# Kernel optimization log

Hardware: AMD Instinct MI355X
Metric: run time of the kernel (lower is better)

The kernel has to match this reference:

```python
import jax, jax.numpy as jnp
import numpy as np
import math

B, L = 2048, 60
D, H, NL = 80, 8, 3
HD = D // H            # head_dim = 10
NLOC, NUSR = 1187, 46
DFF = 2 * D
IN_DIM = D + 24 + 32 + 2   # loc(80)+user(24)+weekday(16)+hour(16)+2 continuous


def _ln(x, g, b):
    m = jnp.mean(x, -1, keepdims=True)
    v = jnp.mean((x - m) ** 2, -1, keepdims=True)
    return (x - m) * jax.lax.rsqrt(v + 1e-5) * g + b


def setup_inputs():
    key = jax.random.key(0)
    k = lambda i: jax.random.fold_in(key, i)
    g = lambda i, shp, s: jax.random.normal(k(i), shp, dtype=jnp.float32) * s
    inp = {
        "loc_seq": jax.random.randint(k(0), (B, L), 0, NLOC),
        "user_seq": jax.random.randint(k(1), (B, L), 0, NUSR),
        "weekday_seq": jax.random.randint(k(2), (B, L), 0, 8),
        "start_min_seq": jax.random.randint(k(3), (B, L), 0, 1440),
        "dur_seq": jax.random.randint(k(4), (B, L), 0, 600),
        "diff_seq": jax.random.randint(k(5), (B, L), 0, 100),
        "seq_len": jax.random.randint(k(6), (B,), 1, L + 1),
    }
    # embedding tables (padding_idx=0 rows zeroed where the module uses it)
    inp["loc_table"] = g(10, (NLOC, D), 0.02).at[0].set(0.0)
    inp["user_table"] = g(11, (NUSR, 24), 0.02).at[0].set(0.0)
    inp["wk_table"] = g(12, (8, 16), 0.02).at[0].set(0.0)
    inp["hr_table"] = g(13, (25, 16), 0.02)
    inp["in_w"] = g(14, (IN_DIM, D), 0.09)
    inp["in_b"] = jnp.zeros((D,), jnp.float32)
    inp["in_g"] = jnp.ones((D,), jnp.float32)
    inp["in_be"] = jnp.zeros((D,), jnp.float32)
    inp["pos_emb"] = g(15, (1, L, D), 0.02)
    # per-layer stacked params (NL=3 layers)
    inp["qkv_w"] = g(16, (NL, D, 3 * D), 0.09)
    inp["proj_w"] = g(17, (NL, D, D), 0.11)
    inp["proj_b"] = jnp.zeros((NL, D), jnp.float32)
    inp["rel_emb"] = g(18, (NL, 2 * L - 1, HD), 1.0)
    inp["n1_g"] = jnp.ones((NL, D), jnp.float32)
    inp["n1_b"] = jnp.zeros((NL, D), jnp.float32)
    inp["ffn_w1"] = g(19, (NL, D, DFF), 0.09)
    inp["ffn_b1"] = jnp.zeros((NL, DFF), jnp.float32)
    inp["ffn_w2"] = g(20, (NL, DFF, D), 0.09)
    inp["ffn_b2"] = jnp.zeros((NL, D), jnp.float32)
    inp["n2_g"] = jnp.ones((NL, D), jnp.float32)
    inp["n2_b"] = jnp.zeros((NL, D), jnp.float32)
    inp["fn_g"] = jnp.ones((D,), jnp.float32)
    inp["fn_b"] = jnp.zeros((D,), jnp.float32)
    inp["pr_w1"] = g(21, (D, D), 0.11)
    inp["pr_b1"] = jnp.zeros((D,), jnp.float32)
    inp["pr_w2"] = g(22, (D, NLOC), 0.04)
    inp["pr_b2"] = jnp.zeros((NLOC,), jnp.float32)
    inp["protos"] = g(23, (NLOC, D), 0.04)
    inp["temp"] = jnp.asarray(2.0, jnp.float32)
    return inp


def reference(loc_seq, user_seq, weekday_seq, start_min_seq, dur_seq, diff_seq, seq_len,
              loc_table, user_table, wk_table, hr_table, in_w, in_b, in_g, in_be, pos_emb,
              qkv_w, proj_w, proj_b, rel_emb, n1_g, n1_b, ffn_w1, ffn_b1, ffn_w2, ffn_b2,
              n2_g, n2_b, fn_g, fn_b, pr_w1, pr_b1, pr_w2, pr_b2, protos, temp):
    Bx, Lx = loc_seq.shape
    loc_e = loc_table[loc_seq]                                            # [B,L,80]
    user_e = jnp.broadcast_to(user_table[user_seq[:, 0]][:, None, :], (Bx, Lx, 24))
    hour = jnp.clip(start_min_seq // 60, 0, 23)
    cont = jnp.stack([diff_seq.astype(jnp.float32) / 10.0,
                      dur_seq.astype(jnp.float32) / 300.0], -1)           # [B,L,2]
    x = jnp.concatenate([loc_e, user_e, wk_table[weekday_seq], hr_table[hour], cont], -1)
    x = _ln(x @ in_w + in_b, in_g, in_be) + pos_emb[:, :Lx, :]
    key_mask = loc_seq == 0                                               # mask keys [B,L]
    pos_idx = jnp.arange(Lx)[None, :] - jnp.arange(Lx)[:, None] + (Lx - 1)  # [L,L]
    scale = 1.0 / math.sqrt(HD)
    for l in range(NL):
        qkv = (x @ qkv_w[l]).reshape(Bx, Lx, 3, H, HD)
        q = qkv[:, :, 0].transpose(0, 2, 1, 3)                            # [B,H,L,hd]
        kk = qkv[:, :, 1].transpose(0, 2, 1, 3)
        v = qkv[:, :, 2].transpose(0, 2, 1, 3)
        rel = rel_emb[l][pos_idx]                                         # [L,L,hd]
        attn = (jnp.einsum('bhid,bhjd->bhij', q, kk)
                + jnp.einsum('bhid,ijd->bhij', q, rel)) * scale
        attn = jnp.where(key_mask[:, None, None, :], -jnp.inf, attn)
        a = jax.nn.softmax(attn, -1)
        o = jnp.einsum('bhij,bhjd->bhid', a, v).transpose(0, 2, 1, 3).reshape(Bx, Lx, D)
        x = _ln(x + o @ proj_w[l] + proj_b[l], n1_g[l], n1_b[l])
        f = jax.nn.gelu(x @ ffn_w1[l] + ffn_b1[l], approximate=False) @ ffn_w2[l] + ffn_b2[l]
        x = _ln(x + f, n2_g[l], n2_b[l])
    x = _ln(x, fn_g, fn_b)
    final = x[jnp.arange(Bx), jnp.clip(seq_len - 1, 0, Lx - 1)]           # [B,80]
    logits_param = jax.nn.gelu(final @ pr_w1 + pr_b1, approximate=False) @ pr_w2 + pr_b2
    fnorm = final / jnp.maximum(jnp.linalg.norm(final, axis=-1, keepdims=True), 1e-12)
    pnorm = protos / jnp.maximum(jnp.linalg.norm(protos, axis=-1, keepdims=True), 1e-12)
    logits = 0.5 * logits_param + 0.5 * (fnorm @ pnorm.T) * 15.0
    return logits / jnp.clip(temp, 0.5, 3.0)
```

## Files before the change

### kernel.cpp

```cpp
#include <hip/hip_runtime.h>
#include <hip/hip_bf16.h>
#include <math.h>

#define BB   2048
#define LL   60
#define DD   80
#define HH   8
#define HDD  10
#define NLNUM 3
#define NLOC 1187
#define DFF  160
#define IN_DIM 138
#define RELN 119
#define SCS  68
#define XP   21
#define HP   41
#define VP   35
#define TS   65

__device__ __forceinline__ float gelu_f(float a) {
  float x = fabsf(a) * 0.70710678118654752f;
  float t = 1.0f / (1.0f + 0.3275911f * x);
  float y = t * (0.254829592f + t * (-0.284496736f + t * (1.421413741f +
            t * (-1.453152027f + t * 1.061405429f))));
  float e = 1.0f - y * __expf(-x * x);
  float erf_s = copysignf(e, a);
  return 0.5f * a * (1.0f + erf_s);
}

__global__ __launch_bounds__(256) void k_rprep(
    const float* __restrict__ rel_emb, float* __restrict__ relTg) {
  int idx = blockIdx.x * 256 + threadIdx.x;
  if (idx >= 3600) return;
  int p = idx % 120;
  int d = (idx / 120) % 10;
  int l = idx / 1200;
  float v = 0.0f;
  if (p < RELN) v = rel_emb[l * RELN * HDD + p * HDD + d];
  relTg[idx] = v;
}

__global__ __launch_bounds__(256) void k_embed(
    const int* __restrict__ loc_seq, const int* __restrict__ user_seq,
    const int* __restrict__ wk_seq, const int* __restrict__ sm_seq,
    const int* __restrict__ dur_seq, const int* __restrict__ diff_seq,
    const float* __restrict__ loc_table, const float* __restrict__ user_table,
    const float* __restrict__ wk_table, const float* __restrict__ hr_table,
    const float* __restrict__ in_w, const float* __restrict__ in_b,
    const float* __restrict__ in_g, const float* __restrict__ in_be,
    const float* __restrict__ pos_emb, float* __restrict__ x) {
  int tok0 = blockIdx.x * 48, tid = threadIdx.x;
  __shared__ __align__(16) float vin[48 * VP * 4];
  __shared__ __align__(16) float ws[140 * 80];
  __shared__ float mstd[96];

  float4* vin4 = (float4*)vin;
  float4* ws4  = (float4*)ws;

  for (int i = tid; i < 140 * 20; i += 256) {
    int r = i / 20, c = i % 20;
    float4 v = make_float4(0.0f, 0.0f, 0.0f, 0.0f);
    if (r < IN_DIM) v = *(const float4*)(in_w + r * 80 + c * 4);
    ws4[i] = v;
  }
  for (int i = tid; i < 48 * 35; i += 256) {
    int t = i / 35, s = i % 35;
    int tok = tok0 + t;
    float4 v;
    if (s < 20) {
      int loc = loc_seq[tok];
      v = *(const float4*)(loc_table + (size_t)loc * 80 + s * 4);
    } else if (s < 26) {
      int usr = user_seq[(tok / LL) * LL];
      v = *(const float4*)(user_table + usr * 24 + (s - 20) * 4);
    } else if (s < 30) {
      int wk = wk_seq[tok];
      v = *(const float4*)(wk_table + wk * 16 + (s - 26) * 4);
    } else if (s < 34) {
      int hr = sm_seq[tok] / 60; hr = min(max(hr, 0), 23);
      v = *(const float4*)(hr_table + hr * 16 + (s - 30) * 4);
    } else {
      v.x = (float)diff_seq[tok] / 10.0f;
      v.y = (float)dur_seq[tok] / 300.0f;
      v.z = 0.0f; v.w = 0.0f;
    }
    vin4[t * VP + s] = v;
  }
  __syncthreads();

  int tg = tid / 20, cg = tid % 20, t0 = tg * 4;
  float acc[4][4] = {};
  if (tid < 240) {
    #pragma unroll 7
    for (int iq = 0; iq < 35; iq++) {
      float4 xv[4], wv[4];
      #pragma unroll
      for (int dt = 0; dt < 4; dt++) xv[dt] = vin4[(t0 + dt) * VP + iq];
      #pragma unroll
      for (int di = 0; di < 4; di++) wv[di] = ws4[(iq * 4 + di) * 20 + cg];
      #pragma unroll
      for (int dt = 0; dt < 4; dt++) {
        const float* xp = (const float*)&xv[dt];
        #pragma unroll
        for (int di = 0; di < 4; di++) {
          const float* wp = (const float*)&wv[di];
          #pragma unroll
          for (int dc = 0; dc < 4; dc++) acc[dt][dc] += xp[di] * wp[dc];
        }
      }
    }
  }
  __syncthreads();
  if (tid < 240) {
    float4 bb = *(const float4*)(in_b + cg * 4);
    const float* bp = (const float*)&bb;
    #pragma unroll
    for (int dt = 0; dt < 4; dt++) {
      float4 y;
      y.x = acc[dt][0] + bp[0];
      y.y = acc[dt][1] + bp[1];
      y.z = acc[dt][2] + bp[2];
      y.w = acc[dt][3] + bp[3];
      vin4[(t0 + dt) * VP + cg] = y;
    }
  }
  __syncthreads();
  if (tid < 48) {
    float s = 0.0f, s2 = 0.0f;
    #pragma unroll
    for (int iq = 0; iq < 20; iq++) {
      float4 v = vin4[tid * VP + iq];
      s  += v.x + v.y + v.z + v.w;
      s2 += v.x * v.x + v.y * v.y + v.z * v.z + v.w * v.w;
    }
    float mean = s / 80.0f;
    float var  = fmaxf(s2 / 80.0f - mean * mean, 0.0f);
    mstd[tid] = mean; mstd[48 + tid] = rsqrtf(var + 1e-5f);
  }
  __syncthreads();
  for (int e = tid; e < 960; e += 256) {
    int t = e / 20, c4 = e % 20;
    float4 v = vin4[t * VP + c4];
    float4 gg = *(const float4*)(in_g + c4 * 4);
    float4 bb = *(const float4*)(in_be + c4 * 4);
    float4 pe = *(const float4*)(pos_emb + ((tok0 + t) % LL) * 80 + c4 * 4);
    float m = mstd[t], r = mstd[48 + t];
    float4 out;
    out.x = (v.x - m) * r * gg.x + bb.x + pe.x;
    out.y = (v.y - m) * r * gg.y + bb.y + pe.y;
    out.z = (v.z - m) * r * gg.z + bb.z + pe.z;
    out.w = (v.w - m) * r * gg.w + bb.w + pe.w;
    ((float4*)(x + (size_t)tok0 * 80))[e] = out;
  }
}

__global__ __launch_bounds__(256) void k_qkv(
    const float* __restrict__ x, const float* __restrict__ qkv_w,
    float* __restrict__ qkvo) {
  int b = blockIdx.x, tid = threadIdx.x;
  __shared__ __align__(16) float xsT[20 * TS * 4];
  __shared__ __align__(16) float ws[80 * 60];

  const float4* xb4 = (const float4*)(x + (size_t)b * 4800);
  float4* xsT4 = (float4*)xsT;
  float4* ws4  = (float4*)ws;
  for (int i = tid; i < 1200; i += 256) {
    int t = i / 20, iq = i % 20;
    xsT4[iq * TS + t] = xb4[i];
  }

  for (int c0 = 0; c0 < 240; c0 += 60) {
    __syncthreads();
    for (int i = tid; i < 1200; i += 256)
      ws4[i] = *(const float4*)(qkv_w + (i / 15) * 240 + c0 + (i % 15) * 4);
    __syncthreads();
    if (tid < 225) {
      int tg = tid % 15, cg = tid / 15;
      int t0 = tg * 4;
      float acc[4][4] = {};
      #pragma unroll 5
      for (int iq = 0; iq < 20; iq++) {
        float4 xv[4], wv[4];
        #pragma unroll
        for (int dt = 0; dt < 4; dt++) xv[dt] = xsT4[iq * TS + t0 + dt];
        #pragma unroll
        for (int di = 0; di < 4; di++) wv[di] = ws4[(iq * 4 + di) * 15 + cg];
        #pragma unroll
        for (int dt = 0; dt < 4; dt++) {
          const float* xp = (const float*)&xv[dt];
          #pragma unroll
          for (int di = 0; di < 4; di++) {
            const float* wp = (const float*)&wv[di];
            #pragma unroll
            for (int dc = 0; dc < 4; dc++) acc[dt][dc] += xp[di] * wp[dc];
          }
        }
      }
      float* qb = qkvo + (size_t)b * 14400 + (size_t)(c0 + cg * 4) * 60 + t0;
      #pragma unroll
      for (int dc = 0; dc < 4; dc++)
        *(float4*)(qb + dc * 60) =
            make_float4(acc[0][dc], acc[1][dc], acc[2][dc], acc[3][dc]);
    }
  }
}

__global__ __launch_bounds__(256) void k_attn(
    const float* __restrict__ qkvo, const int* __restrict__ loc_seq,
    const float* __restrict__ relTg,
    float* __restrict__ o) {
  int bh = blockIdx.x;
  int b = bh >> 3, h = bh & 7;
  int tid = threadIdx.x;

  __shared__ __align__(16) float qs[HDD * 60];
  __shared__ __align__(16) float ks[HDD * 60];
  __shared__ __align__(16) float vs[HDD * 60];
  __shared__ __align__(16) float relT[HDD * 120];
  __shared__ __align__(16) float sc[60 * SCS];
  __shared__ __align__(16) float rsum[64];
  __shared__ float msk[60];

  const float4* src = (const float4*)(qkvo + (size_t)b * 14400);
  float4* q4 = (float4*)qs; float4* k4 = (float4*)ks; float4* v4 = (float4*)vs;
  for (int i = tid; i < 150; i += 256) {
    q4[i] = src[h * 150 + i];
    k4[i] = src[1200 + h * 150 + i];
    v4[i] = src[2400 + h * 150 + i];
  }
  const float4* rg4 = (const float4*)relTg;
  float4* relT4 = (float4*)relT;
  for (int i = tid; i < 300; i += 256) relT4[i] = rg4[i];
  if (tid < 60) msk[tid] = (loc_seq[b * LL + tid] == 0) ? 1.0f : 0.0f;
  __syncthreads();

  if (tid < 225) {
    int ig = tid / 15, jg = tid % 15;
    int i0 = ig * 4, j0 = jg * 4;
    int w0 = j0 - i0 + 56;
    float acc[4][4] = {};
    #pragma unroll
    for (int d = 0; d < 10; d++) {
      float4 qv = *(const float4*)(qs + d * 60 + i0);
      float4 kv = *(const float4*)(ks + d * 60 + j0);
      float4 rA = *(const float4*)(relT + d * 120 + w0);
      float4 rB = *(const float4*)(relT + d * 120 + w0 + 4);
      float rr[8] = {rA.x, rA.y, rA.z, rA.w, rB.x, rB.y, rB.z, rB.w};
      const float* qp = (const float*)&qv;
      const float* kp = (const float*)&kv;
      #pragma unroll
      for (int di = 0; di < 4; di++)
        #pragma unroll
        for (int dj = 0; dj < 4; dj++)
          acc[di][dj] += qp[di] * (kp[dj] + rr[dj - di + 3]);
    }
    const float scale = 0.31622776601683794f;
    #pragma unroll
    for (int di = 0; di < 4; di++) {
      #pragma unroll
      for (int dj = 0; dj < 4; dj++) {
        float v = acc[di][dj] * scale;
        if (msk[j0 + dj] != 0.0f) v = -1e30f;
        acc[di][dj] = v;
      }
      *(float4*)(sc + (i0 + di) * SCS + j0) =
          make_float4(acc[di][0], acc[di][1], acc[di][2], acc[di][3]);
    }
  }
  __syncthreads();

  if (tid < 60) {
    float* row = sc + tid * SCS;
    int c = (tid >> 3) & 7;
    float m0 = -3.0e38f, m1 = -3.0e38f, m2 = -3.0e38f, m3 = -3.0e38f;
    #pragma unroll
    for (int s = 0; s < 15; s++) {
      int k = c + s; if (k >= 15) k -= 15;
      float4 v = *(const float4*)(row + 4 * k);
      m0 = fmaxf(m0, v.x); m1 = fmaxf(m1, v.y);
      m2 = fmaxf(m2, v.z); m3 = fmaxf(m3, v.w);
    }
    float m = fmaxf(fmaxf(m0, m1), fmaxf(m2, m3));
    float s0 = 0.0f, s1 = 0.0f, s2 = 0.0f, s3 = 0.0f;
    #pragma unroll
    for (int s = 0; s < 15; s++) {
      int k = c + s; if (k >= 15) k -= 15;
      float4 v = *(float4*)(row + 4 * k);
      v.x = __expf(v.x - m); v.y = __expf(v.y - m);
      v.z = __expf(v.z - m); v.w = __expf(v.w - m);
      *(float4*)(row + 4 * k) = v;
      s0 += v.x; s1 += v.y; s2 += v.z; s3 += v.w;
    }
    rsum[tid] = 1.0f / (s0 + s1 + s2 + s3);
  }
  __syncthreads();

  if (tid < 150) {
    int ig = tid / 10, d = tid % 10;
    float acc[4] = {0, 0, 0, 0};
    #pragma unroll 5
    for (int jq = 0; jq < 15; jq++) {
      float4 vv = *(const float4*)(vs + d * 60 + jq * 4);
      #pragma unroll
      for (int di = 0; di < 4; di++) {
        float4 av = *(const float4*)(sc + (ig + 15 * di) * SCS + jq * 4);
        acc[di] += av.x * vv.x + av.y * vv.y + av.z * vv.z + av.w * vv.w;
      }
    }
    #pragma unroll
    for (int di = 0; di < 4; di++) {
      float r = rsum[ig + 15 * di];
      o[((size_t)b * 60 + ig + 15 * di) * 80 + h * 10 + d] = acc[di] * r;
    }
  }
}

__global__ __launch_bounds__(256) void k_pffn(
    const float* __restrict__ o, const float* __restrict__ proj_w,
    const float* __restrict__ proj_b, const float* __restrict__ g1,
    const float* __restrict__ be1,
    const float* __restrict__ w1, const float* __restrict__ b1,
    const float* __restrict__ w2, const float* __restrict__ b2,
    const float* __restrict__ g2, const float* __restrict__ be2,
    float* __restrict__ x) {
  int tok0 = blockIdx.x * 48, tid = threadIdx.x;
  __shared__ __align__(16) float ys[48 * XP * 4];
  __shared__ __align__(16) float hs[48 * HP * 4];
  __shared__ __align__(16) float ws[80 * 80];
  __shared__ float mstd[96];

  float4* ys4 = (float4*)ys;
  float4* hs4 = (float4*)hs;
  float4* os4 = (float4*)hs;
  float4* ws4 = (float4*)ws;

  const float4* ob4 = (const float4*)(o + (size_t)tok0 * 80);
  for (int i = tid; i < 960; i += 256) os4[(i / 20) * XP + (i % 20)] = ob4[i];
  for (int i = tid; i < 1600; i += 256)
    ws4[i] = *(const float4*)(proj_w + (i / 20) * 80 + (i % 20) * 4);
  __syncthreads();

  int tg = tid / 20, cg = tid % 20, t0 = tg * 4;
  {
    float acc[4][4] = {};
    if (tid < 240) {
      #pragma unroll
      for (int iq = 0; iq < 20; iq++) {
        float4 xv[4], wv[4];
        #pragma unroll
        for (int dt = 0; dt < 4; dt++) xv[dt] = os4[(t0 + dt) * XP + iq];
        #pragma unroll
        for (int di = 0; di < 4; di++) wv[di] = ws4[(iq * 4 + di) * 20 + cg];
        #pragma unroll
        for (int dt = 0; dt < 4; dt++) {
          const float* xp = (const float*)&xv[dt];
          #pragma unroll
          for (int di = 0; di < 4; di++) {
            const float* wp = (const float*)&wv[di];
            #pragma unroll
            for (int dc = 0; dc < 4; dc++) acc[dt][dc] += xp[di] * wp[dc];
          }
        }
      }
      float4 pb = *(const float4*)(proj_b + cg * 4);
      const float* pbp = (const float*)&pb;
      #pragma unroll
      for (int dt = 0; dt < 4; dt++) {
        float4 xr = *(const float4*)(x + (size_t)(tok0 + t0 + dt) * 80 + cg * 4);
        const float* xrp = (const float*)&xr;
        float4 out;
        out.x = acc[dt][0] + pbp[0] + xrp[0];
        out.y = acc[dt][1] + pbp[1] + xrp[1];
        out.z = acc[dt][2] + pbp[2] + xrp[2];
        out.w = acc[dt][3] + pbp[3] + xrp[3];
        ys4[(t0 + dt) * XP + cg] = out;
      }
    }
  }
  __syncthreads();
  if (tid < 48) {
    float s = 0.0f, s2 = 0.0f;
    #pragma unroll
    for (int iq = 0; iq < 20; iq++) {
      float4 v = ys4[tid * XP + iq];
      s  += v.x + v.y + v.z + v.w;
      s2 += v.x * v.x + v.y * v.y + v.z * v.z + v.w * v.w;
    }
    float mean = s / 80.0f;
    float var  = fmaxf(s2 / 80.0f - mean * mean, 0.0f);
    mstd[tid] = mean; mstd[48 + tid] = rsqrtf(var + 1e-5f);
  }
  __syncthreads();
  for (int e = tid; e < 960; e += 256) {
    int t = e / 20, c4 = e % 20;
    float4 v = ys4[t * XP + c4];
    float4 gg = *(const float4*)(g1 + c4 * 4);
    float4 bb = *(const float4*)(be1 + c4 * 4);
    float m = mstd[t], r = mstd[48 + t];
    v.x = (v.x - m) * r * gg.x + bb.x;
    v.y = (v.y - m) * r * gg.y + bb.y;
    v.z = (v.z - m) * r * gg.z + bb.z;
    v.w = (v.w - m) * r * gg.w + bb.w;
    ys4[t * XP + c4] = v;
  }

  for (int c0 = 0; c0 < 160; c0 += 80) {
    __syncthreads();
    for (int i = tid; i < 1600; i += 256)
      ws4[i] = *(const float4*)(w1 + (i / 20) * 160 + c0 + (i % 20) * 4);
    __syncthreads();
    if (tid < 240) {
      float acc[4][4] = {};
      #pragma unroll
      for (int iq = 0; iq < 20; iq++) {
        float4 xv[4], wv[4];
        #pragma unroll
        for (int dt = 0; dt < 4; dt++) xv[dt] = ys4[(t0 + dt) * XP + iq];
        #pragma unroll
        for (int di = 0; di < 4; di++) wv[di] = ws4[(iq * 4 + di) * 20 + cg];
        #pragma unroll
        for (int dt = 0; dt < 4; dt++) {
          const float* xp = (const float*)&xv[dt];
          #pragma unroll
          for (int di = 0; di < 4; di++) {
            const float* wp = (const float*)&wv[di];
            #pragma unroll
            for (int dc = 0; dc < 4; dc++) acc[dt][dc] += xp[di] * wp[dc];
          }
        }
      }
      float4 bb = *(const float4*)(b1 + c0 + cg * 4);
      const float* bp = (const float*)&bb;
      #pragma unroll
      for (int dt = 0; dt < 4; dt++) {
        float4 out;
        float* op = (float*)&out;
        #pragma unroll
        for (int dc = 0; dc < 4; dc++)
          op[dc] = gelu_f(acc[dt][dc] + bp[dc]);
        hs4[(t0 + dt) * HP + c0 / 4 + cg] = out;
      }
    }
  }

  float acc[4][4] = {};
  for (int k0 = 0; k0 < 160; k0 += 80) {
    __syncthreads();
    for (int i = tid; i < 1600; i += 256)
      ws4[i] = *(const float4*)(w2 + (size_t)(k0 + i / 20) * 80 + (i % 20) * 4);
    __syncthreads();
    if (tid < 240) {
      #pragma unroll
      for (int iq = 0; iq < 20; iq++) {
        float4 hv[4], wv[4];
        #pragma unroll
        for (int dt = 0; dt < 4; dt++) hv[dt] = hs4[(t0 + dt) * HP + k0 / 4 + iq];
        #pragma unroll
        for (int di = 0; di < 4; di++) wv[di] = ws4[(iq * 4 + di) * 20 + cg];
        #pragma unroll
        for (int dt = 0; dt < 4; dt++) {
          const float* hp = (const float*)&hv[dt];
          #pragma unroll
          for (int di = 0; di < 4; di++) {
            const float* wp = (const float*)&wv[di];
            #pragma unroll
            for (int dc = 0; dc < 4; dc++) acc[dt][dc] += hp[di] * wp[dc];
          }
        }
      }
    }
  }
  __syncthreads();
  if (tid < 240) {
    float4 bb = *(const float4*)(b2 + cg * 4);
    const float* bp = (const float*)&bb;
    #pragma unroll
    for (int dt = 0; dt < 4; dt++) {
      float4 xr = ys4[(t0 + dt) * XP + cg];
      const float* xrp = (const float*)&xr;
      float4 out;
      out.x = acc[dt][0] + bp[0] + xrp[0];
      out.y = acc[dt][1] + bp[1] + xrp[1];
      out.z = acc[dt][2] + bp[2] + xrp[2];
      out.w = acc[dt][3] + bp[3] + xrp[3];
      hs4[(t0 + dt) * HP + cg] = out;
    }
  }
  __syncthreads();
  if (tid < 48) {
    float s = 0.0f, s2 = 0.0f;
    #pragma unroll
    for (int iq = 0; iq < 20; iq++) {
      float4 v = hs4[tid * HP + iq];
      s  += v.x + v.y + v.z + v.w;
      s2 += v.x * v.x + v.y * v.y + v.z * v.z + v.w * v.w;
    }
    float mean = s / 80.0f;
    float var  = fmaxf(s2 / 80.0f - mean * mean, 0.0f);
    mstd[tid] = mean; mstd[48 + tid] = rsqrtf(var + 1e-5f);
  }
  __syncthreads();
  for (int e = tid; e < 960; e += 256) {
    int t = e / 20, c4 = e % 20;
    float4 v = hs4[t * HP + c4];
    float4 gg = *(const float4*)(g2 + c4 * 4);
    float4 bb = *(const float4*)(be2 + c4 * 4);
    float m = mstd[t], r = mstd[48 + t];
    float4 out;
    out.x = (v.x - m) * r * gg.x + bb.x;
    out.y = (v.y - m) * r * gg.y + bb.y;
    out.z = (v.z - m) * r * gg.z + bb.z;
    out.w = (v.w - m) * r * gg.w + bb.w;
    ((float4*)(x + (size_t)tok0 * 80))[e] = out;
  }
}

__global__ __launch_bounds__(128) void k_final(
    const float* __restrict__ x, const int* __restrict__ seq_len,
    const float* __restrict__ fn_g, const float* __restrict__ fn_b,
    const float* __restrict__ pr_w1, const float* __restrict__ pr_b1,
    float* __restrict__ fnorm, float* __restrict__ h1) {
  int b = blockIdx.x, tid = threadIdx.x;
  __shared__ float red[128], red2[128];
  __shared__ float fbuf[DD];
  int t = seq_len[b] - 1; t = min(max(t, 0), LL - 1);
  float v = 0.0f;
  if (tid < DD) v = x[((size_t)b * LL + t) * DD + tid];
  red[tid]  = (tid < DD) ? v : 0.0f;
  red2[tid] = (tid < DD) ? v * v : 0.0f;
  __syncthreads();
  for (int s = 64; s > 0; s >>= 1) {
    if (tid < s) { red[tid] += red[tid + s]; red2[tid] += red2[tid + s]; }
    __syncthreads();
  }
  float mean = red[0] / DD;
  float var  = fmaxf(red2[0] / DD - mean * mean, 0.0f);
  float rstd = rsqrtf(var + 1e-5f);
  float f = 0.0f;
  if (tid < DD) { f = (v - mean) * rstd * fn_g[tid] + fn_b[tid]; fbuf[tid] = f; }
  __syncthreads();
  red[tid] = (tid < DD) ? f * f : 0.0f;
  __syncthreads();
  for (int s = 64; s > 0; s >>= 1) {
    if (tid < s) red[tid] += red[tid + s];
    __syncthreads();
  }
  float rn = 1.0f / fmaxf(sqrtf(red[0]), 1e-12f);
  if (tid < DD) {
    fnorm[(size_t)b * DD + tid] = f * rn;
    float gacc = pr_b1[tid];
    for (int i = 0; i < DD; i++) gacc += fbuf[i] * pr_w1[i * DD + tid];
    h1[(size_t)b * DD + tid] = gelu_f(gacc);
  }
}

__global__ __launch_bounds__(128) void k_pnorm(
    const float* __restrict__ protos, float* __restrict__ pnormT) {
  int c = blockIdx.x, tid = threadIdx.x;
  __shared__ float red[128];
  float v = 0.0f;
  if (tid < DD) v = protos[(size_t)c * DD + tid];
  red[tid] = (tid < DD) ? v * v : 0.0f;
  __syncthreads();
  for (int s = 64; s > 0; s >>= 1) {
    if (tid < s) red[tid] += red[tid + s];
    __syncthreads();
  }
  float rn = 1.0f / fmaxf(sqrtf(red[0]), 1e-12f);
  if (tid < DD) pnormT[(size_t)tid * NLOC + c] = v * rn;
}

__global__ __launch_bounds__(256) void k_logits(
    const float* __restrict__ h1, const float* __restrict__ fnorm,
    const float* __restrict__ pr_w2, const float* __restrict__ pr_b2,
    const float* __restrict__ pnormT, const float* __restrict__ temp,
    float* __restrict__ out) {
  int b0 = (blockIdx.x / 5) * 4, cb = blockIdx.x % 5;
  int tid = threadIdx.x;
  int c = cb * 256 + tid;
  __shared__ float h1s[4][DD], fns[4][DD];
  for (int i = tid; i < 4 * DD; i += 256) {
    int j = i / DD, k = i % DD;
    h1s[j][k] = h1[(size_t)(b0 + j) * DD + k];
    fns[j][k] = fnorm[(size_t)(b0 + j) * DD + k];
  }
  __syncthreads();
  if (c < NLOC) {
    float a1[4] = {0, 0, 0, 0}, a2[4] = {0, 0, 0, 0};
    for (int k = 0; k < DD; k++) {
      float w = pr_w2[(size_t)k * NLOC + c];
      float p = pnormT[(size_t)k * NLOC + c];
      #pragma unroll
      for (int j = 0; j < 4; j++) {
        a1[j] += h1s[j][k] * w;
        a2[j] += fns[j][k] * p;
      }
    }
    float pb = pr_b2[c];
    float tt = fminf(fmaxf(temp[0], 0.5f), 3.0f);
    #pragma unroll
    for (int j = 0; j < 4; j++)
      out[(size_t)(b0 + j) * NLOC + c] = (0.5f * (a1[j] + pb) + 7.5f * a2[j]) / tt;
  }
}

extern "C" void kernel_launch(void* const* d_in, const int* in_sizes, int n_in,
                              void* d_out, int out_size, void* d_ws, size_t ws_size,
                              hipStream_t stream) {
  const int* loc_seq   = (const int*)d_in[0];
  const int* user_seq  = (const int*)d_in[1];
  const int* wk_seq    = (const int*)d_in[2];
  const int* sm_seq    = (const int*)d_in[3];
  const int* dur_seq   = (const int*)d_in[4];
  const int* diff_seq  = (const int*)d_in[5];
  const int* seq_len   = (const int*)d_in[6];
  const float* loc_table = (const float*)d_in[7];
  const float* user_table= (const float*)d_in[8];
  const float* wk_table  = (const float*)d_in[9];
  const float* hr_table  = (const float*)d_in[10];
  const float* in_w   = (const float*)d_in[11];
  const float* in_b   = (const float*)d_in[12];
  const float* in_g   = (const float*)d_in[13];
  const float* in_be  = (const float*)d_in[14];
  const float* pos_emb= (const float*)d_in[15];
  const float* qkv_w  = (const float*)d_in[16];
  const float* proj_w = (const float*)d_in[17];
  const float* proj_b = (const float*)d_in[18];
  const float* rel_emb= (const float*)d_in[19];
  const float* n1_g   = (const float*)d_in[20];
  const float* n1_b   = (const float*)d_in[21];
  const float* ffn_w1 = (const float*)d_in[22];
  const float* ffn_b1 = (const float*)d_in[23];
  const float* ffn_w2 = (const float*)d_in[24];
  const float* ffn_b2 = (const float*)d_in[25];
  const float* n2_g   = (const float*)d_in[26];
  const float* n2_b   = (const float*)d_in[27];
  const float* fn_g   = (const float*)d_in[28];
  const float* fn_b   = (const float*)d_in[29];
  const float* pr_w1  = (const float*)d_in[30];
  const float* pr_b1  = (const float*)d_in[31];
  const float* pr_w2  = (const float*)d_in[32];
  const float* pr_b2  = (const float*)d_in[33];
  const float* protos = (const float*)d_in[34];
  const float* temp   = (const float*)d_in[35];
  float* out = (float*)d_out;

  float* x      = (float*)d_ws;
  float* o      = x + (size_t)BB * LL * DD;
  float* qkvo   = o + (size_t)BB * LL * DD;
  float* fnorm  = qkvo + (size_t)BB * 14400;
  float* h1     = fnorm + (size_t)BB * DD;
  float* pnormT = h1 + (size_t)BB * DD;
  float* relTg  = pnormT + (size_t)DD * NLOC;

  k_rprep<<<15, 256, 0, stream>>>(rel_emb, relTg);

  k_embed<<<BB * LL / 48, 256, 0, stream>>>(loc_seq, user_seq, wk_seq, sm_seq,
                                            dur_seq, diff_seq, loc_table,
                                            user_table, wk_table, hr_table,
                                            in_w, in_b, in_g, in_be, pos_emb, x);

  for (int l = 0; l < NLNUM; l++) {
    k_qkv<<<BB, 256, 0, stream>>>(x, qkv_w + (size_t)l * 80 * 240, qkvo);
    k_attn<<<BB * HH, 256, 0, stream>>>(qkvo, loc_seq,
                                        relTg + (size_t)l * 1200, o);
    k_pffn<<<BB * LL / 48, 256, 0, stream>>>(
        o, proj_w + (size_t)l * DD * DD, proj_b + (size_t)l * DD,
        n1_g + (size_t)l * DD, n1_b + (size_t)l * DD,
        ffn_w1 + (size_t)l * DD * DFF, ffn_b1 + (size_t)l * DFF,
        ffn_w2 + (size_t)l * DFF * DD, ffn_b2 + (size_t)l * DD,
        n2_g + (size_t)l * DD, n2_b + (size_t)l * DD, x);
  }

  k_pnorm<<<NLOC, 128, 0, stream>>>(protos, pnormT);
  k_final<<<BB, 128, 0, stream>>>(x, seq_len, fn_g, fn_b, pr_w1, pr_b1, fnorm, h1);
  k_logits<<<(BB / 4) * 5, 256, 0, stream>>>(h1, fnorm, pr_w2, pr_b2, pnormT, temp, out);
}
```

Baseline: 1.520 ms.

## Enlarge pffn tile to 192 tokens and interleave FFN hidden chunks

The projection+FFN kernel now handles 192 tokens per block with 512 threads, and each thread computes two 4x4 output tiles so every weight load from shared memory is reused across twice as many tokens. The FFN is restructured to compute one 80-wide hidden chunk, apply GELU, and immediately accumulate its contribution through W2, so the hidden buffer shrinks to 80 columns. This is meant to cut weight staging traffic and shared-memory loads per FLOP. In exchange it uses more registers and shared memory per block and launches fewer blocks (640), which lowers occupancy.

New measurement: 1.528 ms. About the same (+0.5%).

```diff
diff --git a/kernel.cpp b/kernel.cpp
--- a/kernel.cpp
+++ b/kernel.cpp
@@ -14,7 +14,6 @@
 #define RELN 119
 #define SCS  68
 #define XP   21
-#define HP   41
 #define VP   35
 #define TS   65
 
@@ -315,7 +314,7 @@
   }
 }
 
-__global__ __launch_bounds__(256) void k_pffn(
+__global__ __launch_bounds__(512) void k_pffn(
     const float* __restrict__ o, const float* __restrict__ proj_w,
     const float* __restrict__ proj_b, const float* __restrict__ g1,
     const float* __restrict__ be1,
@@ -323,62 +322,76 @@
     const float* __restrict__ w2, const float* __restrict__ b2,
     const float* __restrict__ g2, const float* __restrict__ be2,
     float* __restrict__ x) {
-  int tok0 = blockIdx.x * 48, tid = threadIdx.x;
-  __shared__ __align__(16) float ys[48 * XP * 4];
-  __shared__ __align__(16) float hs[48 * HP * 4];
-  __shared__ __align__(16) float ws[80 * 80];
-  __shared__ float mstd[96];
+  int tok0 = blockIdx.x * 192, tid = threadIdx.x;
+  __shared__ __align__(16) float ys[192 * XP * 4];
+  __shared__ __align__(16) float hs[192 * XP * 4];
+  __shared__ __align__(16) float ws[1600 * 4];
+  __shared__ float mstd[384];
 
   float4* ys4 = (float4*)ys;
   float4* hs4 = (float4*)hs;
-  float4* os4 = (float4*)hs;
   float4* ws4 = (float4*)ws;
+  const float4* w14 = (const float4*)w1;
+  const float4* w24 = (const float4*)w2;
+
+  int tg = tid / 20, cg = tid % 20;
+  int t0 = tg * 4;
+  bool act = tid < 480;
 
   const float4* ob4 = (const float4*)(o + (size_t)tok0 * 80);
-  for (int i = tid; i < 960; i += 256) os4[(i / 20) * XP + (i % 20)] = ob4[i];
-  for (int i = tid; i < 1600; i += 256)
-    ws4[i] = *(const float4*)(proj_w + (i / 20) * 80 + (i % 20) * 4);
-  __syncthreads();
-
-  int tg = tid / 20, cg = tid % 20, t0 = tg * 4;
+  for (int i = tid; i < 3840; i += 512) hs4[(i / 20) * XP + (i % 20)] = ob4[i];
+  for (int i = tid; i < 1600; i += 512) ws4[i] = ((const float4*)proj_w)[i];
+  __syncthreads();
   {
-    float acc[4][4] = {};
-    if (tid < 240) {
-      #pragma unroll
+    float acc[2][4][4] = {};
+    if (act) {
+      #pragma unroll 5
       for (int iq = 0; iq < 20; iq++) {
-        float4 xv[4], wv[4];
-        #pragma unroll
-        for (int dt = 0; dt < 4; dt++) xv[dt] = os4[(t0 + dt) * XP + iq];
+        float4 xv[2][4], wv[4];
+        #pragma unroll
+        for (int dt = 0; dt < 4; dt++) {
+          xv[0][dt] = hs4[(t0 + dt) * XP + iq];
+          xv[1][dt] = hs4[(96 + t0 + dt) * XP + iq];
+        }
         #pragma unroll
         for (int di = 0; di < 4; di++) wv[di] = ws4[(iq * 4 + di) * 20 + cg];
         #pragma unroll
-        for (int dt = 0; dt < 4; dt++) {
-          const float* xp = (const float*)&xv[dt];
+        for (int u = 0; u < 2; u++)
           #pragma unroll
-          for (int di = 0; di < 4; di++) {
-            const float* wp = (const float*)&wv[di];
+          for (int dt = 0; dt < 4; dt++) {
+            const float* xp = (const float*)&xv[u][dt];
             #pragma unroll
-            for (int dc = 0; dc < 4; dc++) acc[dt][dc] += xp[di] * wp[dc];
+            for (int di = 0; di < 4; di++) {
+              const float* wp = (const float*)&wv[di];
+              #pragma unroll
+              for (int dc = 0; dc < 4; dc++) acc[u][dt][dc] += xp[di] * wp[dc];
+            }
           }
-        }
-      }
+      }
+    }
+    __syncthreads();
+    if (act) {
       float4 pb = *(const float4*)(proj_b + cg * 4);
       const float* pbp = (const float*)&pb;
       #pragma unroll
-      for (int dt = 0; dt < 4; dt++) {
-        float4 xr = *(const float4*)(x + (size_t)(tok0 + t0 + dt) * 80 + cg * 4);
-        const float* xrp = (const float*)&xr;
-        float4 out;
-        out.x = acc[dt][0] + pbp[0] + xrp[0];
-        out.y = acc[dt][1] + pbp[1] + xrp[1];
-        out.z = acc[dt][2] + pbp[2] + xrp[2];
-        out.w = acc[dt][3] + pbp[3] + xrp[3];
-        ys4[(t0 + dt) * XP + cg] = out;
-      }
-    }
-  }
-  __syncthreads();
-  if (tid < 48) {
+      for (int u = 0; u < 2; u++) {
+        int tb = u * 96 + t0;
+        #pragma unroll
+        for (int dt = 0; dt < 4; dt++) {
+          float4 xr = *(const float4*)(x + (size_t)(tok0 + tb + dt) * 80 + cg * 4);
+          const float* xrp = (const float*)&xr;
+          float4 out;
+          out.x = acc[u][dt][0] + pbp[0] + xrp[0];
+          out.y = acc[u][dt][1] + pbp[1] + xrp[1];
+          out.z = acc[u][dt][2] + pbp[2] + xrp[2];
+          out.w = acc[u][dt][3] + pbp[3] + xrp[3];
+          ys4[(tb + dt) * XP + cg] = out;
+        }
+      }
+    }
+  }
+  __syncthreads();
+  if (tid < 192) {
     float s = 0.0f, s2 = 0.0f;
     #pragma unroll
     for (int iq = 0; iq < 20; iq++) {
@@ -388,15 +401,15 @@
     }
     float mean = s / 80.0f;
     float var  = fmaxf(s2 / 80.0f - mean * mean, 0.0f);
-    mstd[tid] = mean; mstd[48 + tid] = rsqrtf(var + 1e-5f);
-  }
-  __syncthreads();
-  for (int e = tid; e < 960; e += 256) {
+    mstd[tid] = mean; mstd[192 + tid] = rsqrtf(var + 1e-5f);
+  }
+  __syncthreads();
+  for (int e = tid; e < 3840; e += 512) {
     int t = e / 20, c4 = e % 20;
     float4 v = ys4[t * XP + c4];
     float4 gg = *(const float4*)(g1 + c4 * 4);
     float4 bb = *(const float4*)(be1 + c4 * 4);
-    float m = mstd[t], r = mstd[48 + t];
+    float m = mstd[t], r = mstd[192 + t];
     v.x = (v.x - m) * r * gg.x + bb.x;
     v.y = (v.y - m) * r * gg.y + bb.y;
     v.z = (v.z - m) * r * gg.z + bb.z;
@@ -404,108 +417,124 @@
     ys4[t * XP + c4] = v;
   }
 
-  for (int c0 = 0; c0 < 160; c0 += 80) {
-    __syncthreads();
-    for (int i = tid; i < 1600; i += 256)
-      ws4[i] = *(const float4*)(w1 + (i / 20) * 160 + c0 + (i % 20) * 4);
-    __syncthreads();
-    if (tid < 240) {
-      float acc[4][4] = {};
-      #pragma unroll
+  float accC[2][4][4] = {};
+  for (int hc = 0; hc < 2; hc++) {
+    __syncthreads();
+    for (int i = tid; i < 1600; i += 512)
+      ws4[i] = w14[(i / 20) * 40 + hc * 20 + (i % 20)];
+    __syncthreads();
+    if (act) {
+      float acc[2][4][4] = {};
+      #pragma unroll 5
       for (int iq = 0; iq < 20; iq++) {
-        float4 xv[4], wv[4];
-        #pragma unroll
-        for (int dt = 0; dt < 4; dt++) xv[dt] = ys4[(t0 + dt) * XP + iq];
+        float4 xv[2][4], wv[4];
+        #pragma unroll
+        for (int dt = 0; dt < 4; dt++) {
+          xv[0][dt] = ys4[(t0 + dt) * XP + iq];
+          xv[1][dt] = ys4[(96 + t0 + dt) * XP + iq];
+        }
         #pragma unroll
         for (int di = 0; di < 4; di++) wv[di] = ws4[(iq * 4 + di) * 20 + cg];
         #pragma unroll
+        for (int u = 0; u < 2; u++)
+          #pragma unroll
+          for (int dt = 0; dt < 4; dt++) {
+            const float* xp = (const float*)&xv[u][dt];
+            #pragma unroll
+            for (int di = 0; di < 4; di++) {
+              const float* wp = (const float*)&wv[di];
+              #pragma unroll
+              for (int dc = 0; dc < 4; dc++) acc[u][dt][dc] += xp[di] * wp[dc];
+            }
+          }
+      }
+      float4 bb = *(const float4*)(b1 + hc * 80 + cg * 4);
+      const float* bp = (const float*)&bb;
+      #pragma unroll
+      for (int u = 0; u < 2; u++) {
+        int tb = u * 96 + t0;
+        #pragma unroll
         for (int dt = 0; dt < 4; dt++) {
-          const float* xp = (const float*)&xv[dt];
+          float4 hv;
+          hv.x = gelu_f(acc[u][dt][0] + bp[0]);
+          hv.y = gelu_f(acc[u][dt][1] + bp[1]);
+          hv.z = gelu_f(acc[u][dt][2] + bp[2]);
+          hv.w = gelu_f(acc[u][dt][3] + bp[3]);
+          hs4[(tb + dt) * XP + cg] = hv;
+        }
+      }
+    }
+    __syncthreads();
+    for (int i = tid; i < 1600; i += 512)
+      ws4[i] = w24[(size_t)(hc * 80 + i / 20) * 20 + (i % 20)];
+    __syncthreads();
+    if (act) {
+      #pragma unroll 5
+      for (int iq = 0; iq < 20; iq++) {
+        float4 hv[2][4], wv[4];
+        #pragma unroll
+        for (int dt = 0; dt < 4; dt++) {
+          hv[0][dt] = hs4[(t0 + dt) * XP + iq];
+          hv[1][dt] = hs4[(96 + t0 + dt) * XP + iq];
+        }
+        #pragma unroll
+        for (int di = 0; di < 4; di++) wv[di] = ws4[(iq * 4 + di) * 20 + cg];
+        #pragma unroll
+        for (int u = 0; u < 2; u++)
           #pragma unroll
-          for (int di = 0; di < 4; di++) {
-            const float* wp = (const float*)&wv[di];
+          for (int dt = 0; dt < 4; dt++) {
+            const float* hp = (const float*)&hv[u][dt];
             #pragma unroll
-            for (int dc = 0; dc < 4; dc++) acc[dt][dc] += xp[di] * wp[dc];
+            for (int di = 0; di < 4; di++) {
+              const float* wp = (const float*)&wv[di];
+              #pragma unroll
+              for (int dc = 0; dc < 4; dc++) accC[u][dt][dc] += hp[di] * wp[dc];
+            }
           }
-        }
-      }
-      float4 bb = *(const float4*)(b1 + c0 + cg * 4);
-      const float* bp = (const float*)&bb;
-      #pragma unroll
-      for (int dt = 0; dt < 4; dt++) {
-        float4 out;
-        float* op = (float*)&out;
-        #pragma unroll
-        for (int dc = 0; dc < 4; dc++)
-          op[dc] = gelu_f(acc[dt][dc] + bp[dc]);
-        hs4[(t0 + dt) * HP + c0 / 4 + cg] = out;
-      }
-    }
-  }
-
-  float acc[4][4] = {};
-  for (int k0 = 0; k0 < 160; k0 += 80) {
-    __syncthreads();
-    for (int i = tid; i < 1600; i += 256)
-      ws4[i] = *(const float4*)(w2 + (size_t)(k0 + i / 20) * 80 + (i % 20) * 4);
-    __syncthreads();
-    if (tid < 240) {
-      #pragma unroll
-      for (int iq = 0; iq < 20; iq++) {
-        float4 hv[4], wv[4];
-        #pragma unroll
-        for (int dt = 0; dt < 4; dt++) hv[dt] = hs4[(t0 + dt) * HP + k0 / 4 + iq];
-        #pragma unroll
-        for (int di = 0; di < 4; di++) wv[di] = ws4[(iq * 4 + di) * 20 + cg];
-        #pragma unroll
-        for (int dt = 0; dt < 4; dt++) {
-          const float* hp = (const float*)&hv[dt];
-          #pragma unroll
-          for (int di = 0; di < 4; di++) {
-            const float* wp = (const float*)&wv[di];
-            #pragma unroll
-            for (int dc = 0; dc < 4; dc++) acc[dt][dc] += hp[di] * wp[dc];
-          }
-        }
-      }
-    }
-  }
-  __syncthreads();
-  if (tid < 240) {
+      }
+    }
+  }
+
+  __syncthreads();
+  if (act) {
     float4 bb = *(const float4*)(b2 + cg * 4);
     const float* bp = (const float*)&bb;
     #pragma unroll
-    for (int dt = 0; dt < 4; dt++) {
-      float4 xr = ys4[(t0 + dt) * XP + cg];
-      const float* xrp = (const float*)&xr;
-      float4 out;
-      out.x = acc[dt][0] + bp[0] + xrp[0];
-      out.y = acc[dt][1] + bp[1] + xrp[1];
-      out.z = acc[dt][2] + bp[2] + xrp[2];
-      out.w = acc[dt][3] + bp[3] + xrp[3];
-      hs4[(t0 + dt) * HP + cg] = out;
-    }
-  }
-  __syncthreads();
-  if (tid < 48) {
+    for (int u = 0; u < 2; u++) {
+      int tb = u * 96 + t0;
+      #pragma unroll
+      for (int dt = 0; dt < 4; dt++) {
+        float4 yv = ys4[(tb + dt) * XP + cg];
+        const float* yp = (const float*)&yv;
+        float4 out;
+        out.x = accC[u][dt][0] + bp[0] + yp[0];
+        out.y = accC[u][dt][1] + bp[1] + yp[1];
+        out.z = accC[u][dt][2] + bp[2] + yp[2];
+        out.w = accC[u][dt][3] + bp[3] + yp[3];
+        hs4[(tb + dt) * XP + cg] = out;
+      }
+    }
+  }
+  __syncthreads();
+  if (tid < 192) {
     float s = 0.0f, s2 = 0.0f;
     #pragma unroll
     for (int iq = 0; iq < 20; iq++) {
-      float4 v = hs4[tid * HP + iq];
+      float4 v = hs4[tid * XP + iq];
       s  += v.x + v.y + v.z + v.w;
       s2 += v.x * v.x + v.y * v.y + v.z * v.z + v.w * v.w;
     }
     float mean = s / 80.0f;
     float var  = fmaxf(s2 / 80.0f - mean * mean, 0.0f);
-    mstd[tid] = mean; mstd[48 + tid] = rsqrtf(var + 1e-5f);
-  }
-  __syncthreads();
-  for (int e = tid; e < 960; e += 256) {
+    mstd[tid] = mean; mstd[192 + tid] = rsqrtf(var + 1e-5f);
+  }
+  __syncthreads();
+  for (int e = tid; e < 3840; e += 512) {
     int t = e / 20, c4 = e % 20;
-    float4 v = hs4[t * HP + c4];
+    float4 v = hs4[t * XP + c4];
     float4 gg = *(const float4*)(g2 + c4 * 4);
     float4 bb = *(const float4*)(be2 + c4 * 4);
-    float m = mstd[t], r = mstd[48 + t];
+    float m = mstd[t], r = mstd[192 + t];
     float4 out;
     out.x = (v.x - m) * r * gg.x + bb.x;
     out.y = (v.y - m) * r * gg.y + bb.y;
@@ -664,7 +693,7 @@
     k_qkv<<<BB, 256, 0, stream>>>(x, qkv_w + (size_t)l * 80 * 240, qkvo);
     k_attn<<<BB * HH, 256, 0, stream>>>(qkvo, loc_seq,
                                         relTg + (size_t)l * 1200, o);
-    k_pffn<<<BB * LL / 48, 256, 0, stream>>>(
+    k_pffn<<<BB * LL / 192, 512, 0, stream>>>(
         o, proj_w + (size_t)l * DD * DD, proj_b + (size_t)l * DD,
         n1_g + (size_t)l * DD, n1_b + (size_t)l * DD,
         ffn_w1 + (size_t)l * DD * DFF, ffn_b1 + (size_t)l * DFF,
```
